# Kernel optimization log

Hardware: AMD Instinct MI355X
Metric: run time of the kernel (lower is better)

The kernel has to match this reference:

```python
import jax, jax.numpy as jnp
import numpy as np

CHUNK = 64  # output-column tile to bound the [M, K, CHUNK] intermediate


def _mam(A, B):
    """Multiply-and-max/min 'matmul': C[m,n] = max_k(A[m,k]*B[k,n]) + min_k(A[m,k]*B[k,n]).
    A: [M, K], B: [K, N]. Tiled over N to avoid materializing [M, K, N]."""
    M, K = A.shape
    N = B.shape[1]
    assert N % CHUNK == 0
    # [N/CHUNK, K, CHUNK]
    B_tiles = B.reshape(K, N // CHUNK, CHUNK).transpose(1, 0, 2)

    def step(carry, B_blk):
        # prod: [M, K, CHUNK]
        prod = A[:, :, None] * B_blk[None, :, :]
        out = prod.max(axis=1) + prod.min(axis=1)  # [M, CHUNK]
        return carry, out

    _, tiles = jax.lax.scan(step, 0, B_tiles)  # [N/CHUNK, M, CHUNK]
    return tiles.transpose(1, 0, 2).reshape(M, N)


def setup_inputs() -> dict:
    key = jax.random.key(0)
    k1, k2, k3 = jax.random.split(key, 3)
    M, K, N = 2048, 1024, 1024
    x = jax.random.normal(k1, (M, K), dtype=jnp.float32)
    # torch stores weight as [out_features, in_features]
    weight = jax.random.normal(k2, (N, K), dtype=jnp.float32) * (1.0 / np.sqrt(K))
    bias = jax.random.normal(k3, (N,), dtype=jnp.float32) * (1.0 / np.sqrt(K))
    return {"x": x, "weight": weight, "bias": bias}


def reference(x, weight, bias):
    # beta == 0 (beta=False): forward is MAM(x, W^T) + bias
    C = _mam(x, weight.T)
    return C + bias[None, :]
```

## Files before the change

kernel.cpp:

```cpp
#include <hip/hip_runtime.h>
#include <math.h>


#define TS 64
#define BK 16
#define LDSP 68
#define STRIPF (BK * LDSP)

__device__ __forceinline__ void mam_upd(float& mx, float& mn, float p0, float p1) {
    asm("v_max3_f32 %0, %1, %2, %0" : "+v"(mx) : "v"(p0), "v"(p1));
    asm("v_min3_f32 %0, %1, %2, %0" : "+v"(mn) : "v"(p0), "v"(p1));
}

__global__
__attribute__((amdgpu_flat_work_group_size(256, 256)))
__attribute__((amdgpu_waves_per_eu(2, 2)))
void mam_sk(
    const float* __restrict__ A, const float* __restrict__ W,
    const float* __restrict__ bias, float* __restrict__ C,
    int M, int N, int K)
{
    __shared__ __align__(16) float smem[8 * STRIPF];
    float* cmx = smem;
    float* cmn = smem + TS * TS;

    const int t    = threadIdx.x;
    const int w    = t >> 6;
    const int lane = t & 63;
    const int ty   = lane >> 3;
    const int tx   = lane & 7;
    const int m0   = blockIdx.y * TS;
    const int n0   = blockIdx.x * TS;
    const int kc   = K >> 2;
    const int kb0  = w * kc;

    const int sr = lane >> 2;
    const int sc = lane & 3;

    float* sAw = smem + (size_t)w * STRIPF;
    float* sWw = smem + (size_t)(4 + w) * STRIPF;

    const float* Ap = A + (size_t)(m0 + sr) * K + kb0 + sc * 4;
    const float* Wp = W + (size_t)(n0 + sr) * K + kb0 + sc * 4;

    float mx[8][8], mn[8][8];
#pragma unroll
    for (int i = 0; i < 8; ++i)
#pragma unroll
        for (int j = 0; j < 8; ++j) {
            mx[i][j] = -INFINITY;
            mn[i][j] =  INFINITY;
        }

    float4 ra[4], rw[4];
#pragma unroll
    for (int q = 0; q < 4; ++q) {
        ra[q] = *(const float4*)(Ap + (size_t)q * 16 * K);
        rw[q] = *(const float4*)(Wp + (size_t)q * 16 * K);
    }
    Ap += BK;
    Wp += BK;

    const int nStages = kc / BK;
    for (int s = 0; s < nStages; ++s) {
#pragma unroll
        for (int q = 0; q < 4; ++q) {
            const int mI = sr + q * 16;
            sAw[(sc * 4 + 0) * LDSP + mI] = ra[q].x;
            sAw[(sc * 4 + 1) * LDSP + mI] = ra[q].y;
            sAw[(sc * 4 + 2) * LDSP + mI] = ra[q].z;
            sAw[(sc * 4 + 3) * LDSP + mI] = ra[q].w;
            sWw[(sc * 4 + 0) * LDSP + mI] = rw[q].x;
            sWw[(sc * 4 + 1) * LDSP + mI] = rw[q].y;
            sWw[(sc * 4 + 2) * LDSP + mI] = rw[q].z;
            sWw[(sc * 4 + 3) * LDSP + mI] = rw[q].w;
        }
        if (s + 1 < nStages) {
#pragma unroll
            for (int q = 0; q < 4; ++q) {
                ra[q] = *(const float4*)(Ap + (size_t)q * 16 * K);
                rw[q] = *(const float4*)(Wp + (size_t)q * 16 * K);
            }
            Ap += BK;
            Wp += BK;
        }

#pragma unroll
        for (int k = 0; k < BK; k += 2) {
            float4 a00 = *(const float4*)&sAw[(k    ) * LDSP + ty * 8];
            float4 a01 = *(const float4*)&sAw[(k    ) * LDSP + ty * 8 + 4];
            float4 a10 = *(const float4*)&sAw[(k + 1) * LDSP + ty * 8];
            float4 a11 = *(const float4*)&sAw[(k + 1) * LDSP + ty * 8 + 4];
            float4 w00 = *(const float4*)&sWw[(k    ) * LDSP + tx * 8];
            float4 w01 = *(const float4*)&sWw[(k    ) * LDSP + tx * 8 + 4];
            float4 w10 = *(const float4*)&sWw[(k + 1) * LDSP + tx * 8];
            float4 w11 = *(const float4*)&sWw[(k + 1) * LDSP + tx * 8 + 4];

            float a0[8] = {a00.x, a00.y, a00.z, a00.w, a01.x, a01.y, a01.z, a01.w};
            float a1[8] = {a10.x, a10.y, a10.z, a10.w, a11.x, a11.y, a11.z, a11.w};
            float b0[8] = {w00.x, w00.y, w00.z, w00.w, w01.x, w01.y, w01.z, w01.w};
            float b1[8] = {w10.x, w10.y, w10.z, w10.w, w11.x, w11.y, w11.z, w11.w};

#pragma unroll
            for (int i = 0; i < 8; ++i)
#pragma unroll
                for (int j = 0; j < 8; ++j) {
                    float p0 = a0[i] * b0[j];
                    float p1 = a1[i] * b1[j];
                    mam_upd(mx[i][j], mn[i][j], p0, p1);
                }
        }
    }

    __syncthreads();

    for (int rnd = 0; rnd < 4; ++rnd) {
        if (w == rnd) {
#pragma unroll
            for (int i = 0; i < 8; ++i)
#pragma unroll
                for (int j = 0; j < 8; ++j) {
                    const int idx = (ty * 8 + i) * TS + tx * 8 + j;
                    if (rnd == 0) {
                        cmx[idx] = mx[i][j];
                        cmn[idx] = mn[i][j];
                    } else {
                        cmx[idx] = fmaxf(cmx[idx], mx[i][j]);
                        cmn[idx] = fminf(cmn[idx], mn[i][j]);
                    }
                }
        }
        __syncthreads();
    }

    float4 blo = *(const float4*)(bias + n0 + tx * 8);
    float4 bhi = *(const float4*)(bias + n0 + tx * 8 + 4);
#pragma unroll
    for (int i2 = 0; i2 < 2; ++i2) {
        const int i   = w * 2 + i2;
        const int row = ty * 8 + i;
        const int idx = row * TS + tx * 8;
        float4 o0, o1;
        o0.x = cmx[idx + 0] + cmn[idx + 0] + blo.x;
        o0.y = cmx[idx + 1] + cmn[idx + 1] + blo.y;
        o0.z = cmx[idx + 2] + cmn[idx + 2] + blo.z;
        o0.w = cmx[idx + 3] + cmn[idx + 3] + blo.w;
        o1.x = cmx[idx + 4] + cmn[idx + 4] + bhi.x;
        o1.y = cmx[idx + 5] + cmn[idx + 5] + bhi.y;
        o1.z = cmx[idx + 6] + cmn[idx + 6] + bhi.z;
        o1.w = cmx[idx + 7] + cmn[idx + 7] + bhi.w;
        float4* p = (float4*)(C + (size_t)(m0 + row) * N + n0 + tx * 8);
        p[0] = o0;
        p[1] = o1;
    }
}

#define BM 64
#define BN 64
#define FBK 32
#define LDSW 68

__device__ __forceinline__ void mam_upd_fb(float& mx, float& mn, float p0, float p1) {
    float nmx, nmn;
    asm("v_max3_f32 %0, %1, %2, %3" : "=v"(nmx) : "v"(p0), "v"(p1), "v"(mx));
    asm("v_min3_f32 %0, %1, %2, %3" : "=v"(nmn) : "v"(p0), "v"(p1), "v"(mn));
    mx = nmx;
    mn = nmn;
}

__global__ __launch_bounds__(256) void mam_fallback(
    const float* __restrict__ A, const float* __restrict__ W,
    const float* __restrict__ bias, float* __restrict__ C,
    int M, int N, int K)
{
    __shared__ float Asf[FBK][LDSW];
    __shared__ float Wsf[FBK][LDSW];

    const int t  = threadIdx.x;
    const int tx = t & 15;
    const int ty = t >> 4;
    const int m0 = blockIdx.y * BM;
    const int n0 = blockIdx.x * BN;
    const int r  = t >> 3;
    const int kq = t & 7;

    const float* Aptr = A + (size_t)(m0 + r) * K + kq * 4;
    const float* Wptr = W + (size_t)(n0 + r) * K + kq * 4;

    float vmax[4][4], vmin[4][4];
#pragma unroll
    for (int i = 0; i < 4; ++i)
#pragma unroll
        for (int j = 0; j < 4; ++j) {
            vmax[i][j] = -INFINITY;
            vmin[i][j] =  INFINITY;
        }

    for (int k0 = 0; k0 < K; k0 += FBK) {
        float4 a0 = *(const float4*)(Aptr);
        float4 a1 = *(const float4*)(Aptr + (size_t)32 * K);
        float4 w0 = *(const float4*)(Wptr);
        float4 w1 = *(const float4*)(Wptr + (size_t)32 * K);
        Aptr += FBK;
        Wptr += FBK;

        const int kk = kq * 4;
        Asf[kk + 0][r]      = a0.x;
        Asf[kk + 1][r]      = a0.y;
        Asf[kk + 2][r]      = a0.z;
        Asf[kk + 3][r]      = a0.w;
        Asf[kk + 0][r + 32] = a1.x;
        Asf[kk + 1][r + 32] = a1.y;
        Asf[kk + 2][r + 32] = a1.z;
        Asf[kk + 3][r + 32] = a1.w;

        Wsf[kk + 0][r]      = w0.x;
        Wsf[kk + 1][r]      = w0.y;
        Wsf[kk + 2][r]      = w0.z;
        Wsf[kk + 3][r]      = w0.w;
        Wsf[kk + 0][r + 32] = w1.x;
        Wsf[kk + 1][r + 32] = w1.y;
        Wsf[kk + 2][r + 32] = w1.z;
        Wsf[kk + 3][r + 32] = w1.w;

        __syncthreads();

#pragma unroll
        for (int k = 0; k < FBK; k += 2) {
            float4 ta0 = *(const float4*)&Asf[k    ][ty * 4];
            float4 ta1 = *(const float4*)&Asf[k + 1][ty * 4];
            float4 tb0 = *(const float4*)&Wsf[k    ][tx * 4];
            float4 tb1 = *(const float4*)&Wsf[k + 1][tx * 4];

            float a0v[4] = {ta0.x, ta0.y, ta0.z, ta0.w};
            float a1v[4] = {ta1.x, ta1.y, ta1.z, ta1.w};
            float b0v[4] = {tb0.x, tb0.y, tb0.z, tb0.w};
            float b1v[4] = {tb1.x, tb1.y, tb1.z, tb1.w};

#pragma unroll
            for (int i = 0; i < 4; ++i)
#pragma unroll
                for (int j = 0; j < 4; ++j) {
                    float p0 = a0v[i] * b0v[j];
                    float p1 = a1v[i] * b1v[j];
                    mam_upd_fb(vmax[i][j], vmin[i][j], p0, p1);
                }
        }
        __syncthreads();
    }

    float4 bv = *(const float4*)(bias + n0 + tx * 4);
#pragma unroll
    for (int i = 0; i < 4; ++i) {
        float4 o;
        o.x = vmax[i][0] + vmin[i][0] + bv.x;
        o.y = vmax[i][1] + vmin[i][1] + bv.y;
        o.z = vmax[i][2] + vmin[i][2] + bv.z;
        o.w = vmax[i][3] + vmin[i][3] + bv.w;
        *(float4*)(C + (size_t)(m0 + ty * 4 + i) * N + n0 + tx * 4) = o;
    }
}

extern "C" void kernel_launch(void* const* d_in, const int* in_sizes, int n_in,
                              void* d_out, int out_size, void* d_ws, size_t ws_size,
                              hipStream_t stream) {
    const float* x    = (const float*)d_in[0];
    const float* w    = (const float*)d_in[1];
    const float* bias = (const float*)d_in[2];
    float* out = (float*)d_out;

    const int N = in_sizes[2];
    const int K = in_sizes[1] / N;
    const int M = in_sizes[0] / K;

    const bool fast_ok = (K % (4 * BK) == 0) && (M % TS == 0) && (N % TS == 0);

    if (fast_ok) {
        dim3 grid(N / TS, M / TS);
        mam_sk<<<grid, 256, 0, stream>>>(x, w, bias, out, M, N, K);
    } else {
        dim3 grid(N / BN, M / BM);
        mam_fallback<<<grid, 256, 0, stream>>>(x, w, bias, out, M, N, K);
    }
}
```

Before: 151.8 us.

## Shrink tile to 64x32 and read weights directly from global into registers

The fast kernel's output tile shrinks from 64x64 to 64x32, and W is no longer staged through LDS. Each thread loads float2 pairs of four W rows straight from global memory, prefetching one k-pair ahead, while only A goes through a per-wave LDS strip. The grid doubles, LDS use halves, per-thread accumulators drop from 128 to 64, and launch bounds now target 4 blocks per CU, all aimed at higher occupancy. In exchange, each thread issues many small uncoalesced-stride global loads of W, and there is less reuse per loaded A value.

After: 318.8 us. +110.0%, slower.

```diff
diff --git a/kernel.cpp b/kernel.cpp
--- a/kernel.cpp
+++ b/kernel.cpp
@@ -2,7 +2,6 @@
 #include <math.h>
 
 
-#define TS 64
 #define BK 16
 #define LDSP 68
 #define STRIPF (BK * LDSP)
@@ -12,103 +11,101 @@
     asm("v_min3_f32 %0, %1, %2, %0" : "+v"(mn) : "v"(p0), "v"(p1));
 }
 
-__global__
-__attribute__((amdgpu_flat_work_group_size(256, 256)))
-__attribute__((amdgpu_waves_per_eu(2, 2)))
-void mam_sk(
+__global__ __launch_bounds__(256, 4) void mam_sk(
     const float* __restrict__ A, const float* __restrict__ W,
     const float* __restrict__ bias, float* __restrict__ C,
     int M, int N, int K)
 {
-    __shared__ __align__(16) float smem[8 * STRIPF];
+    __shared__ __align__(16) float smem[4 * STRIPF];
     float* cmx = smem;
-    float* cmn = smem + TS * TS;
+    float* cmn = smem + 2048;
 
     const int t    = threadIdx.x;
     const int w    = t >> 6;
     const int lane = t & 63;
     const int ty   = lane >> 3;
     const int tx   = lane & 7;
-    const int m0   = blockIdx.y * TS;
-    const int n0   = blockIdx.x * TS;
+    const int m0   = blockIdx.y * 64;
+    const int n0   = blockIdx.x * 32;
     const int kc   = K >> 2;
     const int kb0  = w * kc;
-
-    const int sr = lane >> 2;
-    const int sc = lane & 3;
-
-    float* sAw = smem + (size_t)w * STRIPF;
-    float* sWw = smem + (size_t)(4 + w) * STRIPF;
-
-    const float* Ap = A + (size_t)(m0 + sr) * K + kb0 + sc * 4;
-    const float* Wp = W + (size_t)(n0 + sr) * K + kb0 + sc * 4;
-
-    float mx[8][8], mn[8][8];
+    const int npairs = kc >> 1;
+
+    float* sAw = smem + w * STRIPF;
+
+    const float* Ap = A + (size_t)(m0 + lane) * K + kb0;
+    const float* Wb = W + (size_t)(n0 + tx * 4) * K + kb0;
+
+    float mx[8][4], mn[8][4];
 #pragma unroll
     for (int i = 0; i < 8; ++i)
 #pragma unroll
-        for (int j = 0; j < 8; ++j) {
-            mx[i][j] = -INFINITY;
-            mn[i][j] =  INFINITY;
-        }
-
-    float4 ra[4], rw[4];
-#pragma unroll
-    for (int q = 0; q < 4; ++q) {
-        ra[q] = *(const float4*)(Ap + (size_t)q * 16 * K);
-        rw[q] = *(const float4*)(Wp + (size_t)q * 16 * K);
-    }
-    Ap += BK;
-    Wp += BK;
+        for (int c = 0; c < 4; ++c) {
+            mx[i][c] = -INFINITY;
+            mn[i][c] =  INFINITY;
+        }
+
+    float2 wc[4], wn[4];
+#pragma unroll
+    for (int c = 0; c < 4; ++c)
+        wc[c] = *(const float2*)(Wb + (size_t)c * K);
 
     const int nStages = kc / BK;
     for (int s = 0; s < nStages; ++s) {
-#pragma unroll
-        for (int q = 0; q < 4; ++q) {
-            const int mI = sr + q * 16;
-            sAw[(sc * 4 + 0) * LDSP + mI] = ra[q].x;
-            sAw[(sc * 4 + 1) * LDSP + mI] = ra[q].y;
-            sAw[(sc * 4 + 2) * LDSP + mI] = ra[q].z;
-            sAw[(sc * 4 + 3) * LDSP + mI] = ra[q].w;
-            sWw[(sc * 4 + 0) * LDSP + mI] = rw[q].x;
-            sWw[(sc * 4 + 1) * LDSP + mI] = rw[q].y;
-            sWw[(sc * 4 + 2) * LDSP + mI] = rw[q].z;
-            sWw[(sc * 4 + 3) * LDSP + mI] = rw[q].w;
-        }
-        if (s + 1 < nStages) {
-#pragma unroll
-            for (int q = 0; q < 4; ++q) {
-                ra[q] = *(const float4*)(Ap + (size_t)q * 16 * K);
-                rw[q] = *(const float4*)(Wp + (size_t)q * 16 * K);
+        float4 st0 = *(const float4*)(Ap + 0);
+        float4 st1 = *(const float4*)(Ap + 4);
+        float4 st2 = *(const float4*)(Ap + 8);
+        float4 st3 = *(const float4*)(Ap + 12);
+        Ap += BK;
+        sAw[ 0 * LDSP + lane] = st0.x;
+        sAw[ 1 * LDSP + lane] = st0.y;
+        sAw[ 2 * LDSP + lane] = st0.z;
+        sAw[ 3 * LDSP + lane] = st0.w;
+        sAw[ 4 * LDSP + lane] = st1.x;
+        sAw[ 5 * LDSP + lane] = st1.y;
+        sAw[ 6 * LDSP + lane] = st1.z;
+        sAw[ 7 * LDSP + lane] = st1.w;
+        sAw[ 8 * LDSP + lane] = st2.x;
+        sAw[ 9 * LDSP + lane] = st2.y;
+        sAw[10 * LDSP + lane] = st2.z;
+        sAw[11 * LDSP + lane] = st2.w;
+        sAw[12 * LDSP + lane] = st3.x;
+        sAw[13 * LDSP + lane] = st3.y;
+        sAw[14 * LDSP + lane] = st3.z;
+        sAw[15 * LDSP + lane] = st3.w;
+
+#pragma unroll
+        for (int kp = 0; kp < BK / 2; ++kp) {
+            const int jn = (s * 8 + kp + 1) & (npairs - 1);
+#pragma unroll
+            for (int c = 0; c < 4; ++c)
+                wn[c] = *(const float2*)(Wb + (size_t)c * K + 2 * jn);
+
+            const int k = kp * 2;
+            float4 a0lo = *(const float4*)&sAw[(k    ) * LDSP + ty * 8];
+            float4 a0hi = *(const float4*)&sAw[(k    ) * LDSP + ty * 8 + 4];
+            float4 a1lo = *(const float4*)&sAw[(k + 1) * LDSP + ty * 8];
+            float4 a1hi = *(const float4*)&sAw[(k + 1) * LDSP + ty * 8 + 4];
+
+            float a0[8] = {a0lo.x, a0lo.y, a0lo.z, a0lo.w,
+                           a0hi.x, a0hi.y, a0hi.z, a0hi.w};
+            float a1[8] = {a1lo.x, a1lo.y, a1lo.z, a1lo.w,
+                           a1hi.x, a1hi.y, a1hi.z, a1hi.w};
+
+#pragma unroll
+            for (int c = 0; c < 4; ++c) {
+                const float w0 = wc[c].x;
+                const float w1 = wc[c].y;
+#pragma unroll
+                for (int i = 0; i < 8; ++i) {
+                    float p0 = a0[i] * w0;
+                    float p1 = a1[i] * w1;
+                    mam_upd(mx[i][c], mn[i][c], p0, p1);
+                }
             }
-            Ap += BK;
-            Wp += BK;
-        }
-
-#pragma unroll
-        for (int k = 0; k < BK; k += 2) {
-            float4 a00 = *(const float4*)&sAw[(k    ) * LDSP + ty * 8];
-            float4 a01 = *(const float4*)&sAw[(k    ) * LDSP + ty * 8 + 4];
-            float4 a10 = *(const float4*)&sAw[(k + 1) * LDSP + ty * 8];
-            float4 a11 = *(const float4*)&sAw[(k + 1) * LDSP + ty * 8 + 4];
-            float4 w00 = *(const float4*)&sWw[(k    ) * LDSP + tx * 8];
-            float4 w01 = *(const float4*)&sWw[(k    ) * LDSP + tx * 8 + 4];
-            float4 w10 = *(const float4*)&sWw[(k + 1) * LDSP + tx * 8];
-            float4 w11 = *(const float4*)&sWw[(k + 1) * LDSP + tx * 8 + 4];
-
-            float a0[8] = {a00.x, a00.y, a00.z, a00.w, a01.x, a01.y, a01.z, a01.w};
-            float a1[8] = {a10.x, a10.y, a10.z, a10.w, a11.x, a11.y, a11.z, a11.w};
-            float b0[8] = {w00.x, w00.y, w00.z, w00.w, w01.x, w01.y, w01.z, w01.w};
-            float b1[8] = {w10.x, w10.y, w10.z, w10.w, w11.x, w11.y, w11.z, w11.w};
-
-#pragma unroll
-            for (int i = 0; i < 8; ++i)
-#pragma unroll
-                for (int j = 0; j < 8; ++j) {
-                    float p0 = a0[i] * b0[j];
-                    float p1 = a1[i] * b1[j];
-                    mam_upd(mx[i][j], mn[i][j], p0, p1);
-                }
+#pragma unroll
+            for (int c = 0; c < 4; ++c)
+                wc[c] = wn[c];
         }
     }
 
@@ -119,37 +116,40 @@
 #pragma unroll
             for (int i = 0; i < 8; ++i)
 #pragma unroll
-                for (int j = 0; j < 8; ++j) {
-                    const int idx = (ty * 8 + i) * TS + tx * 8 + j;
+                for (int c = 0; c < 4; ++c) {
+                    const int idx = (ty * 8 + i) * 32 + tx * 4 + c;
                     if (rnd == 0) {
-                        cmx[idx] = mx[i][j];
-                        cmn[idx] = mn[i][j];
+                        cmx[idx] = mx[i][c];
+                        cmn[idx] = mn[i][c];
                     } else {
-                        cmx[idx] = fmaxf(cmx[idx], mx[i][j]);
-                        cmn[idx] = fminf(cmn[idx], mn[i][j]);
+                        cmx[idx] = fmaxf(cmx[idx], mx[i][c]);
+                        cmn[idx] = fminf(cmn[idx], mn[i][c]);
                     }
                 }
         }
         __syncthreads();
     }
 
-    float4 blo = *(const float4*)(bias + n0 + tx * 8);
-    float4 bhi = *(const float4*)(bias + n0 + tx * 8 + 4);
-#pragma unroll
-    for (int i2 = 0; i2 < 2; ++i2) {
-        const int i   = w * 2 + i2;
-        const int row = ty * 8 + i;
-        const int idx = row * TS + tx * 8;
+    {
+        const int r  = t >> 2;
+        const int cg = t & 3;
+        const int idx = r * 32 + cg * 8;
+        float4 x0 = *(const float4*)&cmx[idx];
+        float4 x1 = *(const float4*)&cmx[idx + 4];
+        float4 n0v = *(const float4*)&cmn[idx];
+        float4 n1v = *(const float4*)&cmn[idx + 4];
+        float4 b0 = *(const float4*)(bias + n0 + cg * 8);
+        float4 b1 = *(const float4*)(bias + n0 + cg * 8 + 4);
         float4 o0, o1;
-        o0.x = cmx[idx + 0] + cmn[idx + 0] + blo.x;
-        o0.y = cmx[idx + 1] + cmn[idx + 1] + blo.y;
-        o0.z = cmx[idx + 2] + cmn[idx + 2] + blo.z;
-        o0.w = cmx[idx + 3] + cmn[idx + 3] + blo.w;
-        o1.x = cmx[idx + 4] + cmn[idx + 4] + bhi.x;
-        o1.y = cmx[idx + 5] + cmn[idx + 5] + bhi.y;
-        o1.z = cmx[idx + 6] + cmn[idx + 6] + bhi.z;
-        o1.w = cmx[idx + 7] + cmn[idx + 7] + bhi.w;
-        float4* p = (float4*)(C + (size_t)(m0 + row) * N + n0 + tx * 8);
+        o0.x = x0.x + n0v.x + b0.x;
+        o0.y = x0.y + n0v.y + b0.y;
+        o0.z = x0.z + n0v.z + b0.z;
+        o0.w = x0.w + n0v.w + b0.w;
+        o1.x = x1.x + n1v.x + b1.x;
+        o1.y = x1.y + n1v.y + b1.y;
+        o1.z = x1.z + n1v.z + b1.z;
+        o1.w = x1.w + n1v.w + b1.w;
+        float4* p = (float4*)(C + (size_t)(m0 + r) * N + n0 + cg * 8);
         p[0] = o0;
         p[1] = o1;
     }
@@ -273,10 +273,10 @@
     const int K = in_sizes[1] / N;
     const int M = in_sizes[0] / K;
 
-    const bool fast_ok = (K % (4 * BK) == 0) && (M % TS == 0) && (N % TS == 0);
+    const bool fast_ok = (K % 64 == 0) && (M % 64 == 0) && (N % 32 == 0);
 
     if (fast_ok) {
-        dim3 grid(N / TS, M / TS);
+        dim3 grid(N / 32, M / 64);
         mam_sk<<<grid, 256, 0, stream>>>(x, w, bias, out, M, N, K);
     } else {
         dim3 grid(N / BN, M / BM);
```
